# Kernel optimization log

Measured on AMD Instinct MI355X. Metric: run time of the kernel, lower is better.

The kernel has to match this reference:

```python
import jax, jax.numpy as jnp
import numpy as np


def _apply_ry(state, theta, i, n):
    # state: [B, 2^n] complex; theta: scalar or [B]
    B = state.shape[0]
    s = state.reshape(B, 2**i, 2, 2**(n - i - 1))
    th = jnp.reshape(theta, (-1, 1, 1)) * 0.5
    c, sn = jnp.cos(th), jnp.sin(th)
    a0, a1 = s[:, :, 0], s[:, :, 1]
    return jnp.stack([c * a0 - sn * a1, sn * a0 + c * a1], axis=2).reshape(B, -1)


def _apply_rz(state, theta, i, n):
    B = state.shape[0]
    s = state.reshape(B, 2**i, 2, 2**(n - i - 1))
    ph = jnp.exp(-0.5j * jnp.reshape(theta, (-1, 1, 1)).astype(jnp.float32))
    return jnp.stack([s[:, :, 0] * ph, s[:, :, 1] * jnp.conj(ph)], axis=2).reshape(B, -1)


def _apply_cnot(state, c, t, n):
    # CNOT(control=c, target=t); flips target amplitudes on control=1 slice
    B = state.shape[0]
    s = state.reshape((B,) + (2,) * n)
    ax_c, ax_t = 1 + c, 1 + t
    zero = jnp.take(s, 0, axis=ax_c)
    one = jnp.take(s, 1, axis=ax_c)
    one = jnp.flip(one, axis=ax_t - (1 if t > c else 0))
    return jnp.stack([zero, one], axis=ax_c).reshape(B, -1)


def _z_signs(n):
    # signs[i, k] = +1 if bit i of basis index k is 0 else -1 (qubit 0 = MSB)
    idx = np.arange(2**n)
    bits = (idx[None, :] >> (n - 1 - np.arange(n))[:, None]) & 1
    return jnp.asarray(1.0 - 2.0 * bits, dtype=jnp.float32)  # [n, 2^n]


def _circuit(q_in, w_ry, w_rz):
    # Batched state-vector simulation of: AngleEmbedding(RY) ->
    # n_layers x (per-qubit RY,RZ + CNOT ring) -> <Z_i> expectations.
    B, n = q_in.shape
    L = w_ry.shape[0]
    state = jnp.zeros((B, 2**n), jnp.complex64).at[:, 0].set(1.0)
    for i in range(n):  # AngleEmbedding with rotation='Y'
        state = _apply_ry(state, q_in[:, i], i, n)
    for l in range(L):
        for i in range(n):
            state = _apply_ry(state, w_ry[l, i], i, n)
            state = _apply_rz(state, w_rz[l, i], i, n)
        for i in range(n):  # CNOT ring
            state = _apply_cnot(state, i, (i + 1) % n, n)
    probs = jnp.abs(state) ** 2  # [B, 2^n]
    return probs @ _z_signs(n).T  # [B, n] = <Z_i>


def setup_inputs():
    key = jax.random.key(0)
    ks = jax.random.split(key, 6)
    B, D, n, L = 4096, 512, 10, 4
    return {
        "x": jax.random.normal(ks[0], (B, D), jnp.float32),
        "pre_w": jax.random.normal(ks[1], (n, D), jnp.float32) / np.sqrt(D).astype(np.float32),
        "pre_b": jnp.zeros((n,), jnp.float32),
        "post_w": jax.random.normal(ks[2], (1, n), jnp.float32) / np.sqrt(n).astype(np.float32),
        "post_b": jnp.zeros((1,), jnp.float32),
        "w_ry": jax.random.normal(ks[3], (L, n), jnp.float32),
        "w_rz": jax.random.normal(ks[4], (L, n), jnp.float32),
    }


def reference(x, pre_w, pre_b, post_w, post_b, w_ry, w_rz):
    q_in = x @ pre_w.T + pre_b      # pre_net: [B, n_qubits] rotation angles
    z = _circuit(q_in, w_ry, w_rz)  # [B, n_qubits] PauliZ expectations
    return z @ post_w.T + post_b    # post_net: [B, 1] logits
```

## Files before the change

### kernel.cpp

```cpp
#include <hip/hip_runtime.h>

#define DEV static __device__ __forceinline__

template <int CTRL>
DEV float dpp_xor(float v) {
    int i = __float_as_int(v);
    i = __builtin_amdgcn_update_dpp(i, i, CTRL, 0xF, 0xF, false);
    return __int_as_float(i);
}
template <int PAT>
DEV float swz(float v) {
    return __int_as_float(__builtin_amdgcn_ds_swizzle(__float_as_int(v), PAT));
}
DEV float bperm(int byteaddr, float v) {
    return __int_as_float(__builtin_amdgcn_ds_bpermute(byteaddr, __float_as_int(v)));
}

template <int MASK>
DEV float lanexor(float v, int a32) {
    if constexpr (MASK == 1)       return dpp_xor<0xB1>(v);
    else if constexpr (MASK == 2)  return dpp_xor<0x4E>(v);
    else if constexpr (MASK == 8)  return dpp_xor<0x128>(v);
    else if constexpr (MASK == 4)  return swz<0x101F>(v);
    else if constexpr (MASK == 16) return swz<0x401F>(v);
    else                           return bperm(a32, v);
}
template <int MASK>
DEV float2 lanexor2(float2 v, int a32) {
    return make_float2(lanexor<MASK>(v.x, a32), lanexor<MASK>(v.y, a32));
}

DEV float wave_sum(float v, int a32) {
    v += lanexor<1>(v, 0);
    v += lanexor<2>(v, 0);
    v += lanexor<4>(v, 0);
    v += lanexor<8>(v, 0);
    v += lanexor<16>(v, 0);
    v += bperm(a32, v);
    return v;
}

DEV float2 cmul(float2 a, float2 b) {
    return make_float2(a.x * b.x - a.y * b.y, a.x * b.y + a.y * b.x);
}


template <int P>
DEV void ry2(float2 (&A)[16], float2 (&B)[16], float c, float s, int lane, int a32) {
    if constexpr (P >= 4) {
        constexpr int mask = 1 << (P - 4);
        const float sg = (lane & mask) ? s : -s;
#pragma unroll
        for (int r = 0; r < 16; ++r) {
            float2 pa = lanexor2<mask>(A[r], a32);
            float2 pb = lanexor2<mask>(B[r], a32);
            A[r].x = fmaf(c, A[r].x, sg * pa.x);
            A[r].y = fmaf(c, A[r].y, sg * pa.y);
            B[r].x = fmaf(c, B[r].x, sg * pb.x);
            B[r].y = fmaf(c, B[r].y, sg * pb.y);
        }
    } else {
        constexpr int tb = 1 << P;
#pragma unroll
        for (int r = 0; r < 16; ++r) {
            if (!(r & tb)) {
                const int r2 = r | tb;
                float2 a0 = A[r], a1 = A[r2];
                A[r]  = make_float2(fmaf(c, a0.x, -s * a1.x), fmaf(c, a0.y, -s * a1.y));
                A[r2] = make_float2(fmaf(s, a0.x,  c * a1.x), fmaf(s, a0.y,  c * a1.y));
                float2 b0 = B[r], b1 = B[r2];
                B[r]  = make_float2(fmaf(c, b0.x, -s * b1.x), fmaf(c, b0.y, -s * b1.y));
                B[r2] = make_float2(fmaf(s, b0.x,  c * b1.x), fmaf(s, b0.y,  c * b1.y));
            }
        }
    }
}

DEV int g_of(int a) {
    a ^= ((a >> 1) & 1) ? 1 : 0;
    a ^= ((a >> 2) & 1) ? 2 : 0;
    a ^= ((a >> 3) & 1) ? 4 : 0;
    a ^= ((a >> 4) & 1) ? 8 : 0;
    a ^= ((a >> 5) & 1) ? 16 : 0;
    return a;
}

__global__ void dqc_trig_kernel(const float* __restrict__ w_ry,
                                const float* __restrict__ w_rz,
                                float2* __restrict__ trig) {
    int t = threadIdx.x;
    if (t < 80) {
        float ang = (t < 40 ? w_ry[t] : w_rz[t - 40]) * 0.5f;
        trig[t] = make_float2(__cosf(ang), __sinf(ang));
    }
}

__global__ __launch_bounds__(256, 2) void dqc_main_kernel(
    const float* __restrict__ x, const float* __restrict__ pre_w,
    const float* __restrict__ pre_b, const float* __restrict__ post_w,
    const float* __restrict__ post_b, const float2* __restrict__ trig,
    float* __restrict__ out, int B) {
    const int lane = threadIdx.x & 63;
    const int wid = threadIdx.x >> 6;
    const int w = blockIdx.x * 4 + wid;
    const int b0 = w * 2, b1 = w * 2 + 1;
    if (b0 >= B) return;
    const int b1c = (b1 < B) ? b1 : b0;

    const int a32 = (lane ^ 32) << 2;
    const int h0 = lane ^ ((lane & 1) ? 32 : 0);
    const int cA = g_of(h0) << 2;
    const int cB = g_of(h0 ^ 32) << 2;

    float thA[10], thB[10];
#pragma unroll
    for (int i = 0; i < 10; ++i) { thA[i] = 0.f; thB[i] = 0.f; }
    const float4* xa4 = (const float4*)(x + (size_t)b0 * 512);
    const float4* xb4 = (const float4*)(x + (size_t)b1c * 512);
#pragma unroll
    for (int k = 0; k < 2; ++k) {
        const int vi = lane + 64 * k;
        float4 xva = xa4[vi];
        float4 xvb = xb4[vi];
#pragma unroll
        for (int i = 0; i < 10; ++i) {
            float4 wv = ((const float4*)(pre_w + i * 512))[vi];
            thA[i] = fmaf(xva.x, wv.x, thA[i]);
            thB[i] = fmaf(xvb.x, wv.x, thB[i]);
            thA[i] = fmaf(xva.y, wv.y, thA[i]);
            thB[i] = fmaf(xvb.y, wv.y, thB[i]);
            thA[i] = fmaf(xva.z, wv.z, thA[i]);
            thB[i] = fmaf(xvb.z, wv.z, thB[i]);
            thA[i] = fmaf(xva.w, wv.w, thA[i]);
            thB[i] = fmaf(xvb.w, wv.w, thB[i]);
        }
    }
#pragma unroll
    for (int i = 0; i < 10; ++i) {
        thA[i] = wave_sum(thA[i], a32) + pre_b[i];
        thB[i] = wave_sum(thB[i], a32) + pre_b[i];
    }

    float2 A[16], Bst[16];
    {
        float ccA[10], ssA[10], ccB[10], ssB[10];
#pragma unroll
        for (int i = 0; i < 10; ++i) {
            float aa = thA[i] * 0.5f, ab = thB[i] * 0.5f;
            ccA[i] = __cosf(aa); ssA[i] = __sinf(aa);
            ccB[i] = __cosf(ab); ssB[i] = __sinf(ab);
        }
        float lpA = 1.f, lpB = 1.f;
#pragma unroll
        for (int i = 0; i < 6; ++i) {
            const int bit = (lane >> (5 - i)) & 1;
            lpA *= bit ? ssA[i] : ccA[i];
            lpB *= bit ? ssB[i] : ccB[i];
        }
        float hiA[4], loA[4], hiB[4], loB[4];
#pragma unroll
        for (int j = 0; j < 4; ++j) {
            hiA[j] = lpA * ((j >> 1) ? ssA[6] : ccA[6]) * ((j & 1) ? ssA[7] : ccA[7]);
            loA[j] = ((j >> 1) ? ssA[8] : ccA[8]) * ((j & 1) ? ssA[9] : ccA[9]);
            hiB[j] = lpB * ((j >> 1) ? ssB[6] : ccB[6]) * ((j & 1) ? ssB[7] : ccB[7]);
            loB[j] = ((j >> 1) ? ssB[8] : ccB[8]) * ((j & 1) ? ssB[9] : ccB[9]);
        }
#pragma unroll
        for (int r = 0; r < 16; ++r) {
            A[r]   = make_float2(hiA[r >> 2] * loA[r & 3], 0.f);
            Bst[r] = make_float2(hiB[r >> 2] * loB[r & 3], 0.f);
        }
    }

#pragma unroll 1
    for (int l = 0; l < 4; ++l) {
        const float2* tr = trig + l * 10;
        const float2* tz = trig + 40 + l * 10;

        ry2<9>(A, Bst, tr[0].x, tr[0].y, lane, a32);
        ry2<8>(A, Bst, tr[1].x, tr[1].y, lane, a32);
        ry2<7>(A, Bst, tr[2].x, tr[2].y, lane, a32);
        ry2<6>(A, Bst, tr[3].x, tr[3].y, lane, a32);
        ry2<5>(A, Bst, tr[4].x, tr[4].y, lane, a32);
        ry2<4>(A, Bst, tr[5].x, tr[5].y, lane, a32);
        ry2<3>(A, Bst, tr[6].x, tr[6].y, lane, a32);
        ry2<2>(A, Bst, tr[7].x, tr[7].y, lane, a32);
        ry2<1>(A, Bst, tr[8].x, tr[8].y, lane, a32);
        ry2<0>(A, Bst, tr[9].x, tr[9].y, lane, a32);

        float2 pl;
        {
            float2 z0 = tz[0];
            pl = make_float2(z0.x, ((lane >> 5) & 1) ? z0.y : -z0.y);
#pragma unroll
            for (int q = 1; q < 6; ++q) {
                float2 z = tz[q];
                float sq = ((lane >> (5 - q)) & 1) ? z.y : -z.y;
                pl = cmul(pl, make_float2(z.x, sq));
            }
        }
        float2 p67[4], p89[4];
        {
            const float c6 = tz[6].x, s6 = tz[6].y, c7 = tz[7].x, s7 = tz[7].y;
            const float c8 = tz[8].x, s8 = tz[8].y, c9 = tz[9].x, s9 = tz[9].y;
#pragma unroll
            for (int j = 0; j < 4; ++j) {
                float sg6 = (j >> 1) ? s6 : -s6;
                float sg7 = (j & 1) ? s7 : -s7;
                p67[j] = cmul(cmul(make_float2(c6, sg6), make_float2(c7, sg7)), pl);
                float sg8 = (j >> 1) ? s8 : -s8;
                float sg9 = (j & 1) ? s9 : -s9;
                p89[j] = cmul(make_float2(c8, sg8), make_float2(c9, sg9));
            }
        }
#pragma unroll
        for (int r = 0; r < 16; ++r) {
            const int j = r >> 2, k = r & 3;
            A[r]   = cmul(cmul(A[r], p67[j]), p89[k]);
            Bst[r] = cmul(cmul(Bst[r], p67[j]), p89[k]);
        }

#pragma unroll
        for (int r = 0; r < 16; ++r) {
            const int addr = ((0x6996 >> r) & 1) ? cB : cA;
            A[r].x = bperm(addr, A[r].x);
            A[r].y = bperm(addr, A[r].y);
            Bst[r].x = bperm(addr, Bst[r].x);
            Bst[r].y = bperm(addr, Bst[r].y);
        }
        {
            const bool ctrl = (lane & 1) != 0;
#pragma unroll
            for (int r = 0; r < 8; ++r) {
                const int r2 = r | 8;
                float2 t0 = A[r], t1 = A[r2];
                A[r]  = ctrl ? t1 : t0;
                A[r2] = ctrl ? t0 : t1;
                float2 u0 = Bst[r], u1 = Bst[r2];
                Bst[r]  = ctrl ? u1 : u0;
                Bst[r2] = ctrl ? u0 : u1;
            }
        }
#pragma unroll
        for (int r = 0; r < 16; ++r)
            if ((r & 8) && !(r & 4)) {
                const int r2 = r | 4;
                float2 t = A[r]; A[r] = A[r2]; A[r2] = t;
                t = Bst[r]; Bst[r] = Bst[r2]; Bst[r2] = t;
            }
#pragma unroll
        for (int r = 0; r < 16; ++r)
            if ((r & 4) && !(r & 2)) {
                const int r2 = r | 2;
                float2 t = A[r]; A[r] = A[r2]; A[r2] = t;
                t = Bst[r]; Bst[r] = Bst[r2]; Bst[r2] = t;
            }
#pragma unroll
        for (int r = 0; r < 16; ++r)
            if ((r & 2) && !(r & 1)) {
                const int r2 = r | 1;
                float2 t = A[r]; A[r] = A[r2]; A[r2] = t;
                t = Bst[r]; Bst[r] = Bst[r2]; Bst[r2] = t;
            }
    }

    float laneC = 0.f;
#pragma unroll
    for (int j = 0; j < 6; ++j) {
        int bit = (lane >> (5 - j)) & 1;
        laneC += post_w[j] * (1.f - 2.f * (float)bit);
    }
    float accA = 0.f, accB = 0.f;
#pragma unroll
    for (int r = 0; r < 16; ++r) {
        float regC = 0.f;
#pragma unroll
        for (int j = 6; j < 10; ++j) {
            int bit = (r >> (9 - j)) & 1;
            regC += post_w[j] * (1.f - 2.f * (float)bit);
        }
        const float coef = laneC + regC;
        accA = fmaf(fmaf(A[r].x, A[r].x, A[r].y * A[r].y), coef, accA);
        accB = fmaf(fmaf(Bst[r].x, Bst[r].x, Bst[r].y * Bst[r].y), coef, accB);
    }
    accA = wave_sum(accA, a32);
    accB = wave_sum(accB, a32);
    if (lane == 0) {
        out[b0] = accA + post_b[0];
        if (b1 < B) out[b1] = accB + post_b[0];
    }
}

extern "C" void kernel_launch(void* const* d_in, const int* in_sizes, int n_in,
                              void* d_out, int out_size, void* d_ws, size_t ws_size,
                              hipStream_t stream) {
    const float* x      = (const float*)d_in[0];
    const float* pre_w  = (const float*)d_in[1];
    const float* pre_b  = (const float*)d_in[2];
    const float* post_w = (const float*)d_in[3];
    const float* post_b = (const float*)d_in[4];
    const float* w_ry   = (const float*)d_in[5];
    const float* w_rz   = (const float*)d_in[6];
    float* out = (float*)d_out;
    float2* trig = (float2*)d_ws;

    const int B = in_sizes[0] / 512;

    dqc_trig_kernel<<<1, 128, 0, stream>>>(w_ry, w_rz, trig);
    const int blocks = (B + 7) / 8;
    dqc_main_kernel<<<blocks, 256, 0, stream>>>(x, pre_w, pre_b, post_w,
                                                post_b, trig, out, B);
}
```

Measured before the change: 102.7 us.

## Fold trig precompute into main kernel via shared memory and vectorize complex math

Removes the separate trig kernel launch: each block computes the 80 cos/sin pairs into shared memory after a block barrier, so the early-exit return is replaced by clamped batch indices and guarded stores. Complex arithmetic moves to 2-wide ext_vector floats so the compiler can emit packed FP32 ops (v_pk_fma/v_pk_mul) for the RY rotations. The RZ phase is precombined into a 16-entry table, so each amplitude needs one complex multiply instead of two. Costs are redundant per-block trig work plus a __syncthreads, and a longer prologue holding extra registers.

```diff
diff --git a/kernel.cpp b/kernel.cpp
--- a/kernel.cpp
+++ b/kernel.cpp
@@ -1,6 +1,8 @@
 #include <hip/hip_runtime.h>
 
 #define DEV static __device__ __forceinline__
+
+typedef float f2 __attribute__((ext_vector_type(2)));
 
 template <int CTRL>
 DEV float dpp_xor(float v) {
@@ -26,8 +28,11 @@
     else                           return bperm(a32, v);
 }
 template <int MASK>
-DEV float2 lanexor2(float2 v, int a32) {
-    return make_float2(lanexor<MASK>(v.x, a32), lanexor<MASK>(v.y, a32));
+DEV f2 lanexor2(f2 v, int a32) {
+    f2 r;
+    r.x = lanexor<MASK>(v.x, a32);
+    r.y = lanexor<MASK>(v.y, a32);
+    return r;
 }
 
 DEV float wave_sum(float v, int a32) {
@@ -40,24 +45,31 @@
     return v;
 }
 
-DEV float2 cmul(float2 a, float2 b) {
-    return make_float2(a.x * b.x - a.y * b.y, a.x * b.y + a.y * b.x);
+DEV f2 cmulc(f2 a, f2 b) {
+    f2 r;
+    r.x = a.x * b.x - a.y * b.y;
+    r.y = a.x * b.y + a.y * b.x;
+    return r;
+}
+DEV f2 cmulf2(f2 a, f2 p) {
+    f2 sw;
+    sw.x = -a.y;
+    sw.y = a.x;
+    return p.x * a + p.y * sw;
 }
 
 
 template <int P>
-DEV void ry2(float2 (&A)[16], float2 (&B)[16], float c, float s, int lane, int a32) {
+DEV void ry2(f2 (&A)[16], f2 (&B)[16], float c, float s, int lane, int a32) {
     if constexpr (P >= 4) {
         constexpr int mask = 1 << (P - 4);
         const float sg = (lane & mask) ? s : -s;
 #pragma unroll
         for (int r = 0; r < 16; ++r) {
-            float2 pa = lanexor2<mask>(A[r], a32);
-            float2 pb = lanexor2<mask>(B[r], a32);
-            A[r].x = fmaf(c, A[r].x, sg * pa.x);
-            A[r].y = fmaf(c, A[r].y, sg * pa.y);
-            B[r].x = fmaf(c, B[r].x, sg * pb.x);
-            B[r].y = fmaf(c, B[r].y, sg * pb.y);
+            f2 pa = lanexor2<mask>(A[r], a32);
+            f2 pb = lanexor2<mask>(B[r], a32);
+            A[r] = c * A[r] + sg * pa;
+            B[r] = c * B[r] + sg * pb;
         }
     } else {
         constexpr int tb = 1 << P;
@@ -65,12 +77,12 @@
         for (int r = 0; r < 16; ++r) {
             if (!(r & tb)) {
                 const int r2 = r | tb;
-                float2 a0 = A[r], a1 = A[r2];
-                A[r]  = make_float2(fmaf(c, a0.x, -s * a1.x), fmaf(c, a0.y, -s * a1.y));
-                A[r2] = make_float2(fmaf(s, a0.x,  c * a1.x), fmaf(s, a0.y,  c * a1.y));
-                float2 b0 = B[r], b1 = B[r2];
-                B[r]  = make_float2(fmaf(c, b0.x, -s * b1.x), fmaf(c, b0.y, -s * b1.y));
-                B[r2] = make_float2(fmaf(s, b0.x,  c * b1.x), fmaf(s, b0.y,  c * b1.y));
+                f2 a0 = A[r], a1 = A[r2];
+                A[r]  = c * a0 - s * a1;
+                A[r2] = s * a0 + c * a1;
+                f2 b0 = B[r], b1 = B[r2];
+                B[r]  = c * b0 - s * b1;
+                B[r2] = s * b0 + c * b1;
             }
         }
     }
@@ -85,27 +97,31 @@
     return a;
 }
 
-__global__ void dqc_trig_kernel(const float* __restrict__ w_ry,
-                                const float* __restrict__ w_rz,
-                                float2* __restrict__ trig) {
-    int t = threadIdx.x;
-    if (t < 80) {
-        float ang = (t < 40 ? w_ry[t] : w_rz[t - 40]) * 0.5f;
-        trig[t] = make_float2(__cosf(ang), __sinf(ang));
-    }
-}
-
 __global__ __launch_bounds__(256, 2) void dqc_main_kernel(
     const float* __restrict__ x, const float* __restrict__ pre_w,
     const float* __restrict__ pre_b, const float* __restrict__ post_w,
-    const float* __restrict__ post_b, const float2* __restrict__ trig,
-    float* __restrict__ out, int B) {
+    const float* __restrict__ post_b, const float* __restrict__ w_ry,
+    const float* __restrict__ w_rz, float* __restrict__ out, int B) {
     const int lane = threadIdx.x & 63;
     const int wid = threadIdx.x >> 6;
     const int w = blockIdx.x * 4 + wid;
+
+    __shared__ f2 tt[80];
+    {
+        const int t = threadIdx.x;
+        if (t < 80) {
+            float ang = (t < 40 ? w_ry[t] : w_rz[t - 40]) * 0.5f;
+            f2 z;
+            z.x = __cosf(ang);
+            z.y = __sinf(ang);
+            tt[t] = z;
+        }
+    }
+    __syncthreads();
+
     const int b0 = w * 2, b1 = w * 2 + 1;
-    if (b0 >= B) return;
-    const int b1c = (b1 < B) ? b1 : b0;
+    const int b0c = (b0 < B) ? b0 : B - 1;
+    const int b1c = (b1 < B) ? b1 : B - 1;
 
     const int a32 = (lane ^ 32) << 2;
     const int h0 = lane ^ ((lane & 1) ? 32 : 0);
@@ -115,7 +131,7 @@
     float thA[10], thB[10];
 #pragma unroll
     for (int i = 0; i < 10; ++i) { thA[i] = 0.f; thB[i] = 0.f; }
-    const float4* xa4 = (const float4*)(x + (size_t)b0 * 512);
+    const float4* xa4 = (const float4*)(x + (size_t)b0c * 512);
     const float4* xb4 = (const float4*)(x + (size_t)b1c * 512);
 #pragma unroll
     for (int k = 0; k < 2; ++k) {
@@ -141,7 +157,7 @@
         thB[i] = wave_sum(thB[i], a32) + pre_b[i];
     }
 
-    float2 A[16], Bst[16];
+    f2 A[16], Bs[16];
     {
         float ccA[10], ssA[10], ccB[10], ssB[10];
 #pragma unroll
@@ -167,57 +183,62 @@
         }
 #pragma unroll
         for (int r = 0; r < 16; ++r) {
-            A[r]   = make_float2(hiA[r >> 2] * loA[r & 3], 0.f);
-            Bst[r] = make_float2(hiB[r >> 2] * loB[r & 3], 0.f);
+            A[r].x = hiA[r >> 2] * loA[r & 3];
+            A[r].y = 0.f;
+            Bs[r].x = hiB[r >> 2] * loB[r & 3];
+            Bs[r].y = 0.f;
         }
     }
 
 #pragma unroll 1
     for (int l = 0; l < 4; ++l) {
-        const float2* tr = trig + l * 10;
-        const float2* tz = trig + 40 + l * 10;
-
-        ry2<9>(A, Bst, tr[0].x, tr[0].y, lane, a32);
-        ry2<8>(A, Bst, tr[1].x, tr[1].y, lane, a32);
-        ry2<7>(A, Bst, tr[2].x, tr[2].y, lane, a32);
-        ry2<6>(A, Bst, tr[3].x, tr[3].y, lane, a32);
-        ry2<5>(A, Bst, tr[4].x, tr[4].y, lane, a32);
-        ry2<4>(A, Bst, tr[5].x, tr[5].y, lane, a32);
-        ry2<3>(A, Bst, tr[6].x, tr[6].y, lane, a32);
-        ry2<2>(A, Bst, tr[7].x, tr[7].y, lane, a32);
-        ry2<1>(A, Bst, tr[8].x, tr[8].y, lane, a32);
-        ry2<0>(A, Bst, tr[9].x, tr[9].y, lane, a32);
-
-        float2 pl;
+        const int base = l * 10;
+
+        { f2 z = tt[base + 0]; ry2<9>(A, Bs, z.x, z.y, lane, a32); }
+        { f2 z = tt[base + 1]; ry2<8>(A, Bs, z.x, z.y, lane, a32); }
+        { f2 z = tt[base + 2]; ry2<7>(A, Bs, z.x, z.y, lane, a32); }
+        { f2 z = tt[base + 3]; ry2<6>(A, Bs, z.x, z.y, lane, a32); }
+        { f2 z = tt[base + 4]; ry2<5>(A, Bs, z.x, z.y, lane, a32); }
+        { f2 z = tt[base + 5]; ry2<4>(A, Bs, z.x, z.y, lane, a32); }
+        { f2 z = tt[base + 6]; ry2<3>(A, Bs, z.x, z.y, lane, a32); }
+        { f2 z = tt[base + 7]; ry2<2>(A, Bs, z.x, z.y, lane, a32); }
+        { f2 z = tt[base + 8]; ry2<1>(A, Bs, z.x, z.y, lane, a32); }
+        { f2 z = tt[base + 9]; ry2<0>(A, Bs, z.x, z.y, lane, a32); }
+
+        f2 ptab[16];
         {
-            float2 z0 = tz[0];
-            pl = make_float2(z0.x, ((lane >> 5) & 1) ? z0.y : -z0.y);
+            f2 z0 = tt[40 + base + 0];
+            f2 pl;
+            pl.x = z0.x;
+            pl.y = ((lane >> 5) & 1) ? z0.y : -z0.y;
 #pragma unroll
             for (int q = 1; q < 6; ++q) {
-                float2 z = tz[q];
-                float sq = ((lane >> (5 - q)) & 1) ? z.y : -z.y;
-                pl = cmul(pl, make_float2(z.x, sq));
-            }
-        }
-        float2 p67[4], p89[4];
-        {
-            const float c6 = tz[6].x, s6 = tz[6].y, c7 = tz[7].x, s7 = tz[7].y;
-            const float c8 = tz[8].x, s8 = tz[8].y, c9 = tz[9].x, s9 = tz[9].y;
+                f2 z = tt[40 + base + q];
+                f2 zz;
+                zz.x = z.x;
+                zz.y = ((lane >> (5 - q)) & 1) ? z.y : -z.y;
+                pl = cmulc(pl, zz);
+            }
+            f2 z6 = tt[40 + base + 6], z7 = tt[40 + base + 7];
+            f2 z8 = tt[40 + base + 8], z9 = tt[40 + base + 9];
+            f2 p67[4], p89[4];
 #pragma unroll
             for (int j = 0; j < 4; ++j) {
-                float sg6 = (j >> 1) ? s6 : -s6;
-                float sg7 = (j & 1) ? s7 : -s7;
-                p67[j] = cmul(cmul(make_float2(c6, sg6), make_float2(c7, sg7)), pl);
-                float sg8 = (j >> 1) ? s8 : -s8;
-                float sg9 = (j & 1) ? s9 : -s9;
-                p89[j] = cmul(make_float2(c8, sg8), make_float2(c9, sg9));
-            }
-        }
-#pragma unroll
-        for (int r = 0; r < 16; ++r) {
-            const int j = r >> 2, k = r & 3;
-            A[r]   = cmul(cmul(A[r], p67[j]), p89[k]);
-            Bst[r] = cmul(cmul(Bst[r], p67[j]), p89[k]);
+                f2 a6, a7, a8, a9;
+                a6.x = z6.x; a6.y = (j >> 1) ? z6.y : -z6.y;
+                a7.x = z7.x; a7.y = (j & 1) ? z7.y : -z7.y;
+                p67[j] = cmulc(cmulc(a6, a7), pl);
+                a8.x = z8.x; a8.y = (j >> 1) ? z8.y : -z8.y;
+                a9.x = z9.x; a9.y = (j & 1) ? z9.y : -z9.y;
+                p89[j] = cmulc(a8, a9);
+            }
+#pragma unroll
+            for (int r = 0; r < 16; ++r) ptab[r] = cmulc(p67[r >> 2], p89[r & 3]);
+        }
+#pragma unroll
+        for (int r = 0; r < 16; ++r) {
+            A[r]  = cmulf2(A[r], ptab[r]);
+            Bs[r] = cmulf2(Bs[r], ptab[r]);
         }
 
 #pragma unroll
@@ -225,42 +246,42 @@
             const int addr = ((0x6996 >> r) & 1) ? cB : cA;
             A[r].x = bperm(addr, A[r].x);
             A[r].y = bperm(addr, A[r].y);
-            Bst[r].x = bperm(addr, Bst[r].x);
-            Bst[r].y = bperm(addr, Bst[r].y);
+            Bs[r].x = bperm(addr, Bs[r].x);
+            Bs[r].y = bperm(addr, Bs[r].y);
         }
         {
             const bool ctrl = (lane & 1) != 0;
 #pragma unroll
             for (int r = 0; r < 8; ++r) {
                 const int r2 = r | 8;
-                float2 t0 = A[r], t1 = A[r2];
+                f2 t0 = A[r], t1 = A[r2];
                 A[r]  = ctrl ? t1 : t0;
                 A[r2] = ctrl ? t0 : t1;
-                float2 u0 = Bst[r], u1 = Bst[r2];
-                Bst[r]  = ctrl ? u1 : u0;
-                Bst[r2] = ctrl ? u0 : u1;
+                f2 u0 = Bs[r], u1 = Bs[r2];
+                Bs[r]  = ctrl ? u1 : u0;
+                Bs[r2] = ctrl ? u0 : u1;
             }
         }
 #pragma unroll
         for (int r = 0; r < 16; ++r)
             if ((r & 8) && !(r & 4)) {
                 const int r2 = r | 4;
-                float2 t = A[r]; A[r] = A[r2]; A[r2] = t;
-                t = Bst[r]; Bst[r] = Bst[r2]; Bst[r2] = t;
+                f2 t = A[r]; A[r] = A[r2]; A[r2] = t;
+                t = Bs[r]; Bs[r] = Bs[r2]; Bs[r2] = t;
             }
 #pragma unroll
         for (int r = 0; r < 16; ++r)
             if ((r & 4) && !(r & 2)) {
                 const int r2 = r | 2;
-                float2 t = A[r]; A[r] = A[r2]; A[r2] = t;
-                t = Bst[r]; Bst[r] = Bst[r2]; Bst[r2] = t;
+                f2 t = A[r]; A[r] = A[r2]; A[r2] = t;
+                t = Bs[r]; Bs[r] = Bs[r2]; Bs[r2] = t;
             }
 #pragma unroll
         for (int r = 0; r < 16; ++r)
             if ((r & 2) && !(r & 1)) {
                 const int r2 = r | 1;
-                float2 t = A[r]; A[r] = A[r2]; A[r2] = t;
-                t = Bst[r]; Bst[r] = Bst[r2]; Bst[r2] = t;
+                f2 t = A[r]; A[r] = A[r2]; A[r2] = t;
+                t = Bs[r]; Bs[r] = Bs[r2]; Bs[r2] = t;
             }
     }
 
@@ -281,12 +302,12 @@
         }
         const float coef = laneC + regC;
         accA = fmaf(fmaf(A[r].x, A[r].x, A[r].y * A[r].y), coef, accA);
-        accB = fmaf(fmaf(Bst[r].x, Bst[r].x, Bst[r].y * Bst[r].y), coef, accB);
+        accB = fmaf(fmaf(Bs[r].x, Bs[r].x, Bs[r].y * Bs[r].y), coef, accB);
     }
     accA = wave_sum(accA, a32);
     accB = wave_sum(accB, a32);
     if (lane == 0) {
-        out[b0] = accA + post_b[0];
+        if (b0 < B) out[b0] = accA + post_b[0];
         if (b1 < B) out[b1] = accB + post_b[0];
     }
 }
@@ -302,12 +323,10 @@
     const float* w_ry   = (const float*)d_in[5];
     const float* w_rz   = (const float*)d_in[6];
     float* out = (float*)d_out;
-    float2* trig = (float2*)d_ws;
 
     const int B = in_sizes[0] / 512;
 
-    dqc_trig_kernel<<<1, 128, 0, stream>>>(w_ry, w_rz, trig);
     const int blocks = (B + 7) / 8;
     dqc_main_kernel<<<blocks, 256, 0, stream>>>(x, pre_w, pre_b, post_w,
-                                                post_b, trig, out, B);
-}
+                                                post_b, w_ry, w_rz, out, B);
+}
```

New measurement: 101.2 us. No clear change (-1.5%).
